# Kernel optimization log

Measured on AMD Instinct MI355X. Metric: run time of the kernel, lower is better.

Reference implementation:

```python
import jax, jax.numpy as jnp
import numpy as np

KH = KW = 3
PAD = 1
OFFG = 8  # offset groups: 144 offset channels / (2*9)


def conv2d(x, w, b, pad=PAD):
    out = jax.lax.conv_general_dilated(
        x, w, window_strides=(1, 1), padding=[(pad, pad), (pad, pad)],
        dimension_numbers=('NCHW', 'OIHW', 'NCHW'))
    return out + b[None, :, None, None]


def deform_conv2d(x, offset, w, b):
    # x: [B,C,H,W], offset: [B, 2*K*OFFG, H, W] (per group: (y,x) per kernel tap)
    B, C, H, W = x.shape
    K = KH * KW
    Cg = C // OFFG
    off = offset.reshape(B, OFFG, K, 2, H, W)
    ky, kx = jnp.meshgrid(jnp.arange(KH), jnp.arange(KW), indexing='ij')
    ky = ky.reshape(K).astype(x.dtype)
    kx = kx.reshape(K).astype(x.dtype)
    ys = (jnp.arange(H) - PAD).astype(x.dtype)  # stride 1, dilation 1
    xs = (jnp.arange(W) - PAD).astype(x.dtype)
    # sampling positions [B, OFFG, K, H, W]
    py = ys[None, None, None, :, None] + ky[None, None, :, None, None] + off[:, :, :, 0]
    px = xs[None, None, None, None, :] + kx[None, None, :, None, None] + off[:, :, :, 1]
    y0 = jnp.floor(py)
    x0 = jnp.floor(px)
    xg = x.reshape(B, OFFG, Cg, H * W)
    cols = jnp.zeros((B, OFFG, Cg, K, H, W), x.dtype)
    for dy in (0, 1):
        for dx in (0, 1):
            yi = y0 + dy
            xi = x0 + dx
            wgt = (1.0 - jnp.abs(py - yi)) * (1.0 - jnp.abs(px - xi))
            valid = (yi >= 0) & (yi < H) & (xi >= 0) & (xi < W)
            yc = jnp.clip(yi, 0, H - 1).astype(jnp.int32)
            xc = jnp.clip(xi, 0, W - 1).astype(jnp.int32)
            idx = (yc * W + xc).reshape(B, OFFG, 1, K * H * W)
            g = jnp.take_along_axis(xg, idx, axis=3).reshape(B, OFFG, Cg, K, H, W)
            cols = cols + g * (wgt * valid.astype(x.dtype))[:, :, None]
    cols = cols.reshape(B, C, K, H, W)
    out = jnp.einsum('bckhw,ock->bohw', cols, w.reshape(w.shape[0], C, K))
    return out + b[None, :, None, None]


def setup_inputs() -> dict:
    key = jax.random.key(0)
    ks = jax.random.split(key, 6)
    B, C, H, W = 16, 144, 64, 64
    feat_arm = jax.random.normal(ks[0], (B, C, H, W), jnp.float32)
    feat_up = jax.random.normal(ks[1], (B, C, H, W), jnp.float32)
    # offset conv: in=288 (cat), out=144 = 2*9*OFFG; small init so offsets are sane
    off_w = jax.random.normal(ks[2], (144, 288, 3, 3), jnp.float32) * 0.01
    off_b = jnp.zeros((144,), jnp.float32)
    dcn_w = jax.random.normal(ks[3], (256, 144, 3, 3), jnp.float32) * (1.0 / np.sqrt(144 * 9))
    dcn_b = jnp.zeros((256,), jnp.float32)
    return {'feat_arm': feat_arm, 'feat_up': feat_up, 'off_w': off_w,
            'off_b': off_b, 'dcn_w': dcn_w, 'dcn_b': dcn_b}


def reference(feat_arm, feat_up, off_w, off_b, dcn_w, dcn_b):
    x = jnp.concatenate([feat_arm, feat_up], axis=1)  # [B, 288, H, W]
    offset = conv2d(x, off_w, off_b)                  # [B, 144, H, W]
    y = deform_conv2d(feat_up, offset, dcn_w, dcn_b)  # [B, 256, H, W]
    return jax.nn.silu(y)
```

## Files before the change

### kernel.cpp

```cpp
#include <hip/hip_runtime.h>
#include <math.h>

constexpr int BN = 16;
constexpr int C_IN = 144, C_CAT = 288, C_OFF = 144, C_OUT = 256;
constexpr int OFFG = 8, CG = 18;

constexpr int FUB_ELEMS  = C_IN * BN * 4096;
constexpr int OFFP_ELEMS = BN * 72 * 4096;
constexpr int WOFF_PACK = 9 * 9 * 9 * 512;
constexpr int WDCN_PACK = 8 * 6 * 16 * 512;

typedef __attribute__((ext_vector_type(8))) short bf16x8;
typedef __attribute__((ext_vector_type(4))) float f32x4;
typedef __attribute__((ext_vector_type(4))) unsigned u32x4;

__device__ __forceinline__ unsigned short f2bf(float f) {
  unsigned u = __builtin_bit_cast(unsigned, f);
  return (unsigned short)((u + 0x7FFFu + ((u >> 16) & 1u)) >> 16);
}

__device__ __forceinline__ unsigned packh2(float a, float b) {
  unsigned short ha = __builtin_bit_cast(unsigned short, (_Float16)a);
  unsigned short hb = __builtin_bit_cast(unsigned short, (_Float16)b);
  return (unsigned)ha | ((unsigned)hb << 16);
}
__device__ __forceinline__ float h2f_lo(unsigned u) {
  return (float)__builtin_bit_cast(_Float16, (unsigned short)(u & 0xFFFFu));
}
__device__ __forceinline__ float h2f_hi(unsigned u) {
  return (float)__builtin_bit_cast(_Float16, (unsigned short)(u >> 16));
}
__device__ __forceinline__ float bf_lo(unsigned u) {
  return __builtin_bit_cast(float, u << 16);
}
__device__ __forceinline__ float bf_hi(unsigned u) {
  return __builtin_bit_cast(float, u & 0xFFFF0000u);
}

__device__ __forceinline__ void gload_lds16(const void* g, void* l) {
  __builtin_amdgcn_global_load_lds(
      (const __attribute__((address_space(1))) unsigned*)g,
      (__attribute__((address_space(3))) unsigned*)l, 16, 0, 0);
}

__global__ __launch_bounds__(256) void prep(
    const float* __restrict__ fu, unsigned short* __restrict__ fuB,
    const float* __restrict__ off_w, const float* __restrict__ dcn_w,
    unsigned short* __restrict__ wo, unsigned short* __restrict__ wd) {
  int idx = blockIdx.x * 256 + threadIdx.x;
  int i4 = idx * 4;
  if (i4 < FUB_ELEMS) {
    float4 v = *(const float4*)(fu + i4);
    ushort4 o;
    o.x = f2bf(v.x); o.y = f2bf(v.y); o.z = f2bf(v.z); o.w = f2bf(v.w);
    *(ushort4*)(fuB + i4) = o;
  }
  if (idx < WOFF_PACK) {
    int i = idx & 7, lane = (idx >> 3) & 63, t = idx >> 9;
    int mt = t % 9; t /= 9;
    int tap = t % 9, cb = t / 9;
    int co = mt * 16 + (lane & 15);
    int ci = cb * 32 + ((lane >> 4) << 3) + i;
    wo[idx] = f2bf(off_w[(co * C_CAT + ci) * 9 + tap]);
  }
  if (idx < WDCN_PACK) {
    int i = idx & 7, lane = (idx >> 3) & 63, t = idx >> 9;
    int mt = t & 15; t >>= 4;
    int ks = t % 6, g = t / 6;
    int co = mt * 16 + (lane & 15);
    int r = ks * 32 + ((lane >> 4) << 3) + i;
    float v = 0.f;
    if (r < 162) {
      int ci = r / 9, tap = r - ci * 9;
      v = dcn_w[(co * C_IN + g * CG + ci) * 9 + tap];
    }
    wd[idx] = f2bf(v);
  }
}

__global__ __launch_bounds__(256) void offs_conv_mfma(
    const float* __restrict__ fa, const float* __restrict__ fu,
    const unsigned short* __restrict__ wt, const float* __restrict__ bias,
    unsigned* __restrict__ offp) {
  const int bid = (blockIdx.x & 7) * 64 + (blockIdx.x >> 3);
  const int b = bid >> 5;
  const int y0 = (bid & 31) << 1;
  const int tid = threadIdx.x;
  const int wave = tid >> 6, lane = tid & 63;
  const int kg = lane >> 4, ln = lane & 15;

  __shared__ __align__(16) unsigned short xs[4 * 66 * 32];

  f32x4 acc[9][2];
#pragma unroll
  for (int m = 0; m < 9; ++m)
#pragma unroll
    for (int n = 0; n < 2; ++n) acc[m][n] = {0.f, 0.f, 0.f, 0.f};

  for (int cb = 0; cb < 9; ++cb) {
    __syncthreads();
    for (int idx = tid; idx < 2112; idx += 256) {
      int q = idx / 264;
      int rem = idx - q * 264;
      int row = rem / 66;
      int cc = rem - row * 66;
      int y = y0 - 1 + row, x = cc - 1;
      ushort4 wv = make_ushort4(0, 0, 0, 0);
      if (y >= 0 && y < 64 && x >= 0 && x < 64) {
        int cib = cb * 32 + (q << 2);
        const float* p = (cib < C_IN)
                             ? fa + (((size_t)(b * C_IN + cib)) << 12)
                             : fu + (((size_t)(b * C_IN + cib - C_IN)) << 12);
        int o = (y << 6) + x;
        wv.x = f2bf(p[o]);
        wv.y = f2bf(p[o + 4096]);
        wv.z = f2bf(p[o + 8192]);
        wv.w = f2bf(p[o + 12288]);
      }
      int e = ((row * 66 + cc) << 5) + (((q >> 1) ^ (cc & 3)) << 3) + ((q & 1) << 2);
      *(ushort4*)&xs[e] = wv;
    }
    __syncthreads();

    for (int tap = 0; tap < 9; ++tap) {
      const int ky = tap / 3, kx = tap - ky * 3;
      bf16x8 a[9];
      const unsigned short* wp = wt + (((size_t)(cb * 9 + tap) * 9) << 9) + (lane << 3);
#pragma unroll
      for (int m = 0; m < 9; ++m) a[m] = *(const bf16x8*)(wp + (m << 9));
#pragma unroll
      for (int n = 0; n < 2; ++n) {
        int px = ((wave << 1) + n) * 16 + ln;
        int row = (px >> 6) + ky, cc = (px & 63) + kx;
        int e = ((row * 66 + cc) << 5) + ((kg ^ (cc & 3)) << 3);
        bf16x8 bv = *(const bf16x8*)&xs[e];
#pragma unroll
        for (int m = 0; m < 9; ++m)
          acc[m][n] = __builtin_amdgcn_mfma_f32_16x16x32_bf16(a[m], bv, acc[m][n], 0, 0, 0);
      }
    }
  }

#pragma unroll
  for (int n = 0; n < 2; ++n) {
    int px = ((wave << 1) + n) * 16 + ln;
    int y = y0 + (px >> 6), x = px & 63;
#pragma unroll
    for (int m = 0; m < 9; ++m) {
      int cob = m * 16 + (kg << 2);
#pragma unroll
      for (int rr = 0; rr < 4; rr += 2) {
        unsigned v = packh2(acc[m][n][rr] + bias[cob + rr],
                            acc[m][n][rr + 1] + bias[cob + rr + 1]);
        offp[(((size_t)(b * 72 + ((cob + rr) >> 1))) << 12) + (y << 6) + x] = v;
      }
    }
  }
}

__global__ __launch_bounds__(512, 4) void dcn_mfma(
    const unsigned short* __restrict__ fuB, const unsigned* __restrict__ offp,
    const unsigned short* __restrict__ wt, const float* __restrict__ bias,
    float* __restrict__ out) {
  const int bid = (blockIdx.x & 7) * 128 + (blockIdx.x >> 3);
  const int b = bid >> 6, h = bid & 63;
  const int tid = threadIdx.x;
  const int wave = tid >> 6, lane = tid & 63;
  const int kg = lane >> 4, ln = lane & 15;
  const int wm = wave >> 2, wn = wave & 3;
  const int px = (wn << 4) + ln;

  __shared__ __align__(16) unsigned short colsT[64 * 202];
  __shared__ __align__(16) unsigned short wl[3][8192];

  f32x4 acc[8];
#pragma unroll
  for (int m = 0; m < 8; ++m) acc[m] = {0.f, 0.f, 0.f, 0.f};

  for (int i = tid; i < 64 * 15; i += 512) {
    int p = i / 15, d = i - p * 15;
    *(unsigned*)&colsT[p * 202 + 162 + 2 * d] = 0u;
  }

  {
    const unsigned short* src = wt + (wave * 2) * 512 + lane * 8;
#pragma unroll
    for (int j = 0; j < 2; ++j)
      gload_lds16(src + j * 512, &wl[0][(wave * 2 + j) * 512]);
  }

  auto make_geo = [&](int gg_, int tap, int p) -> uint4 {
    int ky = tap / 3, kx = tap - ky * 3;
    unsigned op = offp[(((size_t)(b * 72 + gg_ * 9 + tap)) << 12) + (h << 6) + p];
    float oy = h2f_lo(op), ox = h2f_hi(op);
    float py = (float)(h - 1 + ky) + oy;
    float pxs = (float)(p - 1 + kx) + ox;
    float y0f = floorf(py), x0f = floorf(pxs);
    int y0 = (int)y0f, x0 = (int)x0f;
    float fy = py - y0f, fx = pxs - x0f;
    float vy0 = (y0 >= 0 && y0 < 64) ? 1.f : 0.f;
    float vy1 = (y0 + 1 >= 0 && y0 + 1 < 64) ? 1.f : 0.f;
    float vx0 = (x0 >= 0 && x0 < 64) ? 1.f : 0.f;
    float vx1 = (x0 + 1 >= 0 && x0 + 1 < 64) ? 1.f : 0.f;
    float a0 = (1.f - fx) * vx0;
    float a1 = fx * vx1;
    float wlo = (x0 == -1) ? a1 : (x0 == 63 ? 0.f : a0);
    float whi = (x0 == 63) ? a0 : (x0 == -1 ? 0.f : a1);
    int xL = min(max(x0, 0), 62);
    int yc0 = min(max(y0, 0), 63), yc1 = min(max(y0 + 1, 0), 63);
    float cy0 = (1.f - fy) * vy0, cy1 = fy * vy1;
    uint4 r;
    r.x = (unsigned)((yc0 << 6) + xL) | ((unsigned)((yc1 << 6) + xL) << 16);
    r.y = 0u;
    r.z = packh2(cy0 * wlo, cy0 * whi);
    r.w = packh2(cy1 * wlo, cy1 * whi);
    return r;
  };

  int tg = 0, cur = 0;
  for (int g = 0; g < OFFG; ++g) {
    __syncthreads();

    uint4 gg = make_geo(g, wave, lane);
    uint4 g8 = make_geo(g, 8, lane);

    const unsigned short* gbase = fuB + (((size_t)(b * C_IN + g * CG)) << 12);
    {
      const int iL0 = gg.x & 0xFFFFu, iL1 = gg.x >> 16;
      const float wl0 = h2f_lo(gg.z), wh0 = h2f_hi(gg.z);
      const float wl1 = h2f_lo(gg.w), wh1 = h2f_hi(gg.w);
      const int j0 = g8.x & 0xFFFFu, j1 = g8.x >> 16;
      const float ul0 = h2f_lo(g8.z), uh0 = h2f_hi(g8.z);
      const float ul1 = h2f_lo(g8.w), uh1 = h2f_hi(g8.w);
      const int n8 = (wave < 2) ? 3 : 2;

      unsigned d0[18], d1[18], e0[3], e1[3];
#pragma unroll
      for (int u = 0; u < 18; ++u) {
        const unsigned short* pl = gbase + ((size_t)u << 12);
        __builtin_memcpy(&d0[u], pl + iL0, 4);
        __builtin_memcpy(&d1[u], pl + iL1, 4);
      }
#pragma unroll
      for (int u = 0; u < 3; ++u) {
        if (u < n8) {
          const unsigned short* pl = gbase + ((size_t)(wave + 8 * u) << 12);
          __builtin_memcpy(&e0[u], pl + j0, 4);
          __builtin_memcpy(&e1[u], pl + j1, 4);
        }
      }
#pragma unroll
      for (int u = 0; u < 18; ++u) {
        float s = wl0 * bf_lo(d0[u]) + wh0 * bf_hi(d0[u]) +
                  wl1 * bf_lo(d1[u]) + wh1 * bf_hi(d1[u]);
        colsT[lane * 202 + u * 9 + wave] = f2bf(s);
      }
#pragma unroll
      for (int u = 0; u < 3; ++u) {
        if (u < n8) {
          float s = ul0 * bf_lo(e0[u]) + uh0 * bf_hi(e0[u]) +
                    ul1 * bf_lo(e1[u]) + uh1 * bf_hi(e1[u]);
          colsT[lane * 202 + (wave + 8 * u) * 9 + 8] = f2bf(s);
        }
      }
    }
    __syncthreads();

    for (int ks = 0; ks < 6; ++ks, ++tg) {
      int cbase = px * 202 + ks * 32 + (kg << 3);
      u32x4 bu;
      bu[0] = *(const unsigned*)&colsT[cbase];
      bu[1] = *(const unsigned*)&colsT[cbase + 2];
      bu[2] = *(const unsigned*)&colsT[cbase + 4];
      bu[3] = *(const unsigned*)&colsT[cbase + 6];
      bf16x8 bv = __builtin_bit_cast(bf16x8, bu);

      int nxt = cur + 1;
      if (nxt == 3) nxt = 0;
      if (tg < 47) {
        const unsigned short* src =
            wt + (size_t)(tg + 1) * 8192 + (wave * 2) * 512 + lane * 8;
        unsigned short* dst = wl[nxt];
#pragma unroll
        for (int j = 0; j < 2; ++j)
          gload_lds16(src + j * 512, dst + (wave * 2 + j) * 512);
        asm volatile("s_waitcnt vmcnt(2)" ::: "memory");
      } else {
        asm volatile("s_waitcnt vmcnt(0)" ::: "memory");
      }
      __builtin_amdgcn_s_barrier();

      const unsigned short* wbuf = wl[cur] + (wm * 8) * 512 + lane * 8;
#pragma unroll
      for (int j = 0; j < 8; ++j) {
        bf16x8 av = *(const bf16x8*)(wbuf + j * 512);
        acc[j] = __builtin_amdgcn_mfma_f32_16x16x32_bf16(av, bv, acc[j], 0, 0, 0);
      }
      cur = nxt;
    }
  }

#pragma unroll
  for (int j = 0; j < 8; ++j) {
    int cob = (wm * 8 + j) * 16 + (kg << 2);
#pragma unroll
    for (int r = 0; r < 4; ++r) {
      float y = acc[j][r] + bias[cob + r];
      out[(((size_t)(b * C_OUT + cob + r)) << 12) + (h << 6) + px] =
          y / (1.f + expf(-y));
    }
  }
}

extern "C" void kernel_launch(void* const* d_in, const int* in_sizes, int n_in,
                              void* d_out, int out_size, void* d_ws, size_t ws_size,
                              hipStream_t stream) {
  const float* feat_arm = (const float*)d_in[0];
  const float* feat_up  = (const float*)d_in[1];
  const float* off_w    = (const float*)d_in[2];
  const float* off_b    = (const float*)d_in[3];
  const float* dcn_w    = (const float*)d_in[4];
  const float* dcn_b    = (const float*)d_in[5];
  float* out = (float*)d_out;

  unsigned short* fuB = (unsigned short*)d_ws;
  unsigned* offp = (unsigned*)(fuB + FUB_ELEMS);
  unsigned short* wo = (unsigned short*)(offp + OFFP_ELEMS);
  unsigned short* wd = wo + WOFF_PACK;

  prep<<<FUB_ELEMS / 1024, 256, 0, stream>>>(feat_up, fuB, off_w, dcn_w, wo, wd);
  offs_conv_mfma<<<BN * 32, 256, 0, stream>>>(feat_arm, feat_up, wo, off_b, offp);
  dcn_mfma<<<BN * 64, 512, 0, stream>>>(fuB, offp, wd, dcn_b, out);
}
```

Baseline: 258.7 us.

## Load DCN weight fragments directly from global memory instead of LDS triple buffer

Drops the LDS triple-buffered async weight prefetch and its per-k-step barrier. Each wave now reads its MFMA A-fragments straight from global memory (relying on L2/L1 reuse across blocks) and partially unrolls the k loop. This removes 48 KB of LDS per block and one barrier per step, which may raise occupancy. The cost is exposed global load latency in front of the MFMAs and more global traffic, because every wave fetches its own weight slice.

Measured after the change: 312.0 us. 1.21x slower.

```diff
diff --git a/kernel.cpp b/kernel.cpp
--- a/kernel.cpp
+++ b/kernel.cpp
@@ -35,12 +35,6 @@
 }
 __device__ __forceinline__ float bf_hi(unsigned u) {
   return __builtin_bit_cast(float, u & 0xFFFF0000u);
-}
-
-__device__ __forceinline__ void gload_lds16(const void* g, void* l) {
-  __builtin_amdgcn_global_load_lds(
-      (const __attribute__((address_space(1))) unsigned*)g,
-      (__attribute__((address_space(3))) unsigned*)l, 16, 0, 0);
 }
 
 __global__ __launch_bounds__(256) void prep(
@@ -171,7 +165,6 @@
   const int px = (wn << 4) + ln;
 
   __shared__ __align__(16) unsigned short colsT[64 * 202];
-  __shared__ __align__(16) unsigned short wl[3][8192];
 
   f32x4 acc[8];
 #pragma unroll
@@ -180,13 +173,6 @@
   for (int i = tid; i < 64 * 15; i += 512) {
     int p = i / 15, d = i - p * 15;
     *(unsigned*)&colsT[p * 202 + 162 + 2 * d] = 0u;
-  }
-
-  {
-    const unsigned short* src = wt + (wave * 2) * 512 + lane * 8;
-#pragma unroll
-    for (int j = 0; j < 2; ++j)
-      gload_lds16(src + j * 512, &wl[0][(wave * 2 + j) * 512]);
   }
 
   auto make_geo = [&](int gg_, int tap, int p) -> uint4 {
@@ -217,7 +203,6 @@
     return r;
   };
 
-  int tg = 0, cur = 0;
   for (int g = 0; g < OFFG; ++g) {
     __syncthreads();
 
@@ -266,7 +251,8 @@
     }
     __syncthreads();
 
-    for (int ks = 0; ks < 6; ++ks, ++tg) {
+#pragma unroll 2
+    for (int ks = 0; ks < 6; ++ks) {
       int cbase = px * 202 + ks * 32 + (kg << 3);
       u32x4 bu;
       bu[0] = *(const unsigned*)&colsT[cbase];
@@ -275,28 +261,14 @@
       bu[3] = *(const unsigned*)&colsT[cbase + 6];
       bf16x8 bv = __builtin_bit_cast(bf16x8, bu);
 
-      int nxt = cur + 1;
-      if (nxt == 3) nxt = 0;
-      if (tg < 47) {
-        const unsigned short* src =
-            wt + (size_t)(tg + 1) * 8192 + (wave * 2) * 512 + lane * 8;
-        unsigned short* dst = wl[nxt];
-#pragma unroll
-        for (int j = 0; j < 2; ++j)
-          gload_lds16(src + j * 512, dst + (wave * 2 + j) * 512);
-        asm volatile("s_waitcnt vmcnt(2)" ::: "memory");
-      } else {
-        asm volatile("s_waitcnt vmcnt(0)" ::: "memory");
-      }
-      __builtin_amdgcn_s_barrier();
-
-      const unsigned short* wbuf = wl[cur] + (wm * 8) * 512 + lane * 8;
-#pragma unroll
-      for (int j = 0; j < 8; ++j) {
-        bf16x8 av = *(const bf16x8*)(wbuf + j * 512);
-        acc[j] = __builtin_amdgcn_mfma_f32_16x16x32_bf16(av, bv, acc[j], 0, 0, 0);
-      }
-      cur = nxt;
+      const unsigned short* wp =
+          wt + (size_t)(g * 6 + ks) * 8192 + (wm * 8) * 512 + lane * 8;
+      bf16x8 a[8];
+#pragma unroll
+      for (int j = 0; j < 8; ++j) a[j] = *(const bf16x8*)(wp + j * 512);
+#pragma unroll
+      for (int j = 0; j < 8; ++j)
+        acc[j] = __builtin_amdgcn_mfma_f32_16x16x32_bf16(a[j], bv, acc[j], 0, 0, 0);
     }
   }
 
```
